# Optimization experiments

Measured on AMD Instinct MI355X. Metric: run time of the kernel, lower is better.

## Reference

```python
import jax, jax.numpy as jnp
import numpy as np

EPS = 1e-07

def setup_inputs() -> dict:
    key = jax.random.key(0)
    k1, k2 = jax.random.split(key)
    B, C = 65536, 1000
    output = jax.random.normal(k1, (B, C), dtype=jnp.float32)
    target = jax.random.randint(k2, (B,), 0, C, dtype=jnp.int64)
    return {"output": output, "target": target}

def reference(output, target):
    B, C = output.shape
    # L2-normalize each row (p=2 norm over class dim) then softmax over classes
    norms = jnp.linalg.norm(output, axis=-1, keepdims=True) + EPS
    probs = jax.nn.softmax(output / norms, axis=1)  # [B, C]
    # per-class mean confidence [C]
    avg_conf = jnp.mean(probs, axis=0)
    # per-class empirical frequency [C] via one-hot-free bincount
    counts = jnp.zeros((C,), dtype=probs.dtype).at[target].add(1.0)
    avg_count = counts / B
    # mean absolute calibration gap over classes (scalar)
    return jnp.mean(jnp.abs(avg_conf - avg_count))
```

## Files before the change

kernel.cpp:

```cpp
#include <hip/hip_runtime.h>
#include <math.h>

#define TPB 512
#define NBLK 1024
#define CCLS 1000

__device__ __forceinline__ float wave_sum64(float x) {
  int t;
  t = __builtin_amdgcn_update_dpp(0, __float_as_int(x), 0x111, 0xf, 0xf, true); x += __int_as_float(t);
  t = __builtin_amdgcn_update_dpp(0, __float_as_int(x), 0x112, 0xf, 0xf, true); x += __int_as_float(t);
  t = __builtin_amdgcn_update_dpp(0, __float_as_int(x), 0x114, 0xf, 0xf, true); x += __int_as_float(t);
  t = __builtin_amdgcn_update_dpp(0, __float_as_int(x), 0x118, 0xf, 0xf, true); x += __int_as_float(t);
  t = __builtin_amdgcn_update_dpp(0, __float_as_int(x), 0x142, 0xa, 0xf, true); x += __int_as_float(t);
  t = __builtin_amdgcn_update_dpp(0, __float_as_int(x), 0x143, 0xc, 0xf, true); x += __int_as_float(t);
  return __int_as_float(__builtin_amdgcn_readlane(__float_as_int(x), 63));
}

__global__ __launch_bounds__(TPB, 8) void mdca_main(const float* __restrict__ X,
                                                    float* __restrict__ g_acc, int B) {
  __shared__ float sacc[1024];
  const int t = threadIdx.x;
  const int lane = t & 63;
  const int wid = blockIdx.x * (TPB / 64) + (t >> 6);
  const int nw = NBLK * (TPB / 64);
  const bool v3 = (lane < 58);

  for (int i = t; i < 1024; i += TPB) sacc[i] = 0.f;

  float acc[16];
  #pragma unroll
  for (int i = 0; i < 16; ++i) acc[i] = 0.f;

  const float4 Z = make_float4(0.f, 0.f, 0.f, 0.f);

  for (int r = wid; r < B; r += nw) {
    const float4* b = reinterpret_cast<const float4*>(X + (size_t)r * CCLS);
    float4 a0 = b[lane];
    float4 a1 = b[64 + lane];
    float4 a2 = b[128 + lane];
    float4 a3 = v3 ? b[192 + lane] : Z;

    float ss = a0.x*a0.x + a0.y*a0.y + a0.z*a0.z + a0.w*a0.w
             + a1.x*a1.x + a1.y*a1.y + a1.z*a1.z + a1.w*a1.w
             + a2.x*a2.x + a2.y*a2.y + a2.z*a2.z + a2.w*a2.w
             + a3.x*a3.x + a3.y*a3.y + a3.z*a3.z + a3.w*a3.w;
    ss = wave_sum64(ss);

    const float inv = 1.0f / (sqrtf(ss) + 1e-7f);

    a0.x=__expf(a0.x*inv); a0.y=__expf(a0.y*inv); a0.z=__expf(a0.z*inv); a0.w=__expf(a0.w*inv);
    a1.x=__expf(a1.x*inv); a1.y=__expf(a1.y*inv); a1.z=__expf(a1.z*inv); a1.w=__expf(a1.w*inv);
    a2.x=__expf(a2.x*inv); a2.y=__expf(a2.y*inv); a2.z=__expf(a2.z*inv); a2.w=__expf(a2.w*inv);
    a3.x=__expf(a3.x*inv); a3.y=__expf(a3.y*inv); a3.z=__expf(a3.z*inv); a3.w=__expf(a3.w*inv);
    if (!v3) a3 = Z;

    float es = a0.x+a0.y+a0.z+a0.w + a1.x+a1.y+a1.z+a1.w
             + a2.x+a2.y+a2.z+a2.w + a3.x+a3.y+a3.z+a3.w;
    es = wave_sum64(es);

    const float invS = 1.0f / es;

    acc[0]  += a0.x*invS;  acc[1]  += a0.y*invS;  acc[2]  += a0.z*invS;  acc[3]  += a0.w*invS;
    acc[4]  += a1.x*invS;  acc[5]  += a1.y*invS;  acc[6]  += a1.z*invS;  acc[7]  += a1.w*invS;
    acc[8]  += a2.x*invS;  acc[9]  += a2.y*invS;  acc[10] += a2.z*invS;  acc[11] += a2.w*invS;
    acc[12] += a3.x*invS;  acc[13] += a3.y*invS;  acc[14] += a3.z*invS;  acc[15] += a3.w*invS;
  }

  __syncthreads();
  #pragma unroll
  for (int k = 0; k < 4; ++k)
    #pragma unroll
    for (int j = 0; j < 4; ++j)
      atomicAdd(&sacc[k * 256 + lane * 4 + j], acc[k * 4 + j]);
  __syncthreads();
  #pragma unroll
  for (int j = 0; j < 2; ++j) {
    int c = t * 2 + j;
    if (c < CCLS) atomicAdd(&g_acc[c], sacc[c]);
  }
}

__global__ __launch_bounds__(256) void mdca_count(const int* __restrict__ tgt,
                                                  float* __restrict__ g_cnt, int B) {
  __shared__ int scnt[CCLS];
  for (int i = threadIdx.x; i < CCLS; i += 256) scnt[i] = 0;
  __syncthreads();
  for (int i = blockIdx.x * 256 + threadIdx.x; i < B; i += gridDim.x * 256)
    atomicAdd(&scnt[tgt[i]], 1);
  __syncthreads();
  for (int i = threadIdx.x; i < CCLS; i += 256) {
    int v = scnt[i];
    if (v) atomicAdd(&g_cnt[i], (float)v);
  }
}

__global__ __launch_bounds__(256) void mdca_final(const float* __restrict__ g_acc,
                                                  const float* __restrict__ g_cnt,
                                                  float* __restrict__ out, int B) {
  __shared__ float s_r[4];
  int t = threadIdx.x;
  float invB = 1.0f / (float)B;
  float s = 0.f;
  for (int c = t; c < CCLS; c += 256)
    s += fabsf((g_acc[c] - g_cnt[c]) * invB);
  #pragma unroll
  for (int off = 32; off > 0; off >>= 1) s += __shfl_down(s, off, 64);
  if ((t & 63) == 0) s_r[t >> 6] = s;
  __syncthreads();
  if (t == 0) out[0] = (s_r[0] + s_r[1] + s_r[2] + s_r[3]) / (float)CCLS;
}

extern "C" void kernel_launch(void* const* d_in, const int* in_sizes, int n_in,
                              void* d_out, int out_size, void* d_ws, size_t ws_size,
                              hipStream_t stream) {
  const float* X = (const float*)d_in[0];
  const int* tgt = (const int*)d_in[1];
  const int B = in_sizes[1];

  float* g_acc = (float*)d_ws;
  float* g_cnt = g_acc + 1024;

  hipMemsetAsync(d_ws, 0, 2048 * sizeof(float), stream);

  mdca_count<<<32, 256, 0, stream>>>(tgt, g_cnt, B);
  mdca_main<<<NBLK, TPB, 0, stream>>>(X, g_acc, B);
  mdca_final<<<1, 256, 0, stream>>>(g_acc, g_cnt, (float*)d_out, B);
}
```

Measured before the change: 380.3 us.

## Fuse count, main and final kernels with last-block reduction; use exp2

```diff
diff --git a/kernel.cpp b/kernel.cpp
--- a/kernel.cpp
+++ b/kernel.cpp
@@ -16,9 +16,25 @@
   return __int_as_float(__builtin_amdgcn_readlane(__float_as_int(x), 63));
 }
 
-__global__ __launch_bounds__(TPB, 8) void mdca_main(const float* __restrict__ X,
-                                                    float* __restrict__ g_acc, int B) {
+__device__ __forceinline__ float fexp2(float x) {
+#if __has_builtin(__builtin_amdgcn_exp2f)
+  return __builtin_amdgcn_exp2f(x);
+#else
+  return exp2f(x);
+#endif
+}
+
+__device__ __forceinline__ float coherent_load(const float* p) {
+  return __hip_atomic_load(p, __ATOMIC_RELAXED, __HIP_MEMORY_SCOPE_AGENT);
+}
+
+__global__ __launch_bounds__(TPB, 8) void mdca_fused(const float* __restrict__ X,
+                                                     const int* __restrict__ tgt,
+                                                     float* __restrict__ g_acc,
+                                                     float* __restrict__ out, int B) {
   __shared__ float sacc[1024];
+  __shared__ float s_r[TPB / 64];
+  __shared__ int s_last;
   const int t = threadIdx.x;
   const int lane = t & 63;
   const int wid = blockIdx.x * (TPB / 64) + (t >> 6);
@@ -46,12 +62,12 @@
              + a3.x*a3.x + a3.y*a3.y + a3.z*a3.z + a3.w*a3.w;
     ss = wave_sum64(ss);
 
-    const float inv = 1.0f / (sqrtf(ss) + 1e-7f);
+    const float il2 = 1.44269504f / (sqrtf(ss) + 1e-7f);
 
-    a0.x=__expf(a0.x*inv); a0.y=__expf(a0.y*inv); a0.z=__expf(a0.z*inv); a0.w=__expf(a0.w*inv);
-    a1.x=__expf(a1.x*inv); a1.y=__expf(a1.y*inv); a1.z=__expf(a1.z*inv); a1.w=__expf(a1.w*inv);
-    a2.x=__expf(a2.x*inv); a2.y=__expf(a2.y*inv); a2.z=__expf(a2.z*inv); a2.w=__expf(a2.w*inv);
-    a3.x=__expf(a3.x*inv); a3.y=__expf(a3.y*inv); a3.z=__expf(a3.z*inv); a3.w=__expf(a3.w*inv);
+    a0.x=fexp2(a0.x*il2); a0.y=fexp2(a0.y*il2); a0.z=fexp2(a0.z*il2); a0.w=fexp2(a0.w*il2);
+    a1.x=fexp2(a1.x*il2); a1.y=fexp2(a1.y*il2); a1.z=fexp2(a1.z*il2); a1.w=fexp2(a1.w*il2);
+    a2.x=fexp2(a2.x*il2); a2.y=fexp2(a2.y*il2); a2.z=fexp2(a2.z*il2); a2.w=fexp2(a2.w*il2);
+    a3.x=fexp2(a3.x*il2); a3.y=fexp2(a3.y*il2); a3.z=fexp2(a3.z*il2); a3.w=fexp2(a3.w*il2);
     if (!v3) a3 = Z;
 
     float es = a0.x+a0.y+a0.z+a0.w + a1.x+a1.y+a1.z+a1.w
@@ -72,42 +88,43 @@
     #pragma unroll
     for (int j = 0; j < 4; ++j)
       atomicAdd(&sacc[k * 256 + lane * 4 + j], acc[k * 4 + j]);
+
+  if (t < 64) {
+    for (int i = blockIdx.x * 64 + t; i < B; i += NBLK * 64)
+      atomicAdd(&sacc[tgt[i]], -1.0f);
+  }
   __syncthreads();
+
   #pragma unroll
   for (int j = 0; j < 2; ++j) {
     int c = t * 2 + j;
     if (c < CCLS) atomicAdd(&g_acc[c], sacc[c]);
   }
-}
 
-__global__ __launch_bounds__(256) void mdca_count(const int* __restrict__ tgt,
-                                                  float* __restrict__ g_cnt, int B) {
-  __shared__ int scnt[CCLS];
-  for (int i = threadIdx.x; i < CCLS; i += 256) scnt[i] = 0;
   __syncthreads();
-  for (int i = blockIdx.x * 256 + threadIdx.x; i < B; i += gridDim.x * 256)
-    atomicAdd(&scnt[tgt[i]], 1);
+  if (t == 0) {
+    __threadfence();
+    unsigned* dcnt = (unsigned*)(g_acc + 1000);
+    unsigned old = __hip_atomic_fetch_add(dcnt, 1u, __ATOMIC_ACQ_REL,
+                                          __HIP_MEMORY_SCOPE_AGENT);
+    s_last = (old == (unsigned)(NBLK - 1));
+  }
   __syncthreads();
-  for (int i = threadIdx.x; i < CCLS; i += 256) {
-    int v = scnt[i];
-    if (v) atomicAdd(&g_cnt[i], (float)v);
+  if (s_last) {
+    const float invB = 1.0f / (float)B;
+    float s = 0.f;
+    for (int c = t; c < CCLS; c += TPB)
+      s += fabsf(coherent_load(&g_acc[c]) * invB);
+    s = wave_sum64(s);
+    if (lane == 0) s_r[t >> 6] = s;
+    __syncthreads();
+    if (t == 0) {
+      float tot = 0.f;
+      #pragma unroll
+      for (int w = 0; w < TPB / 64; ++w) tot += s_r[w];
+      out[0] = tot / (float)CCLS;
+    }
   }
-}
-
-__global__ __launch_bounds__(256) void mdca_final(const float* __restrict__ g_acc,
-                                                  const float* __restrict__ g_cnt,
-                                                  float* __restrict__ out, int B) {
-  __shared__ float s_r[4];
-  int t = threadIdx.x;
-  float invB = 1.0f / (float)B;
-  float s = 0.f;
-  for (int c = t; c < CCLS; c += 256)
-    s += fabsf((g_acc[c] - g_cnt[c]) * invB);
-  #pragma unroll
-  for (int off = 32; off > 0; off >>= 1) s += __shfl_down(s, off, 64);
-  if ((t & 63) == 0) s_r[t >> 6] = s;
-  __syncthreads();
-  if (t == 0) out[0] = (s_r[0] + s_r[1] + s_r[2] + s_r[3]) / (float)CCLS;
 }
 
 extern "C" void kernel_launch(void* const* d_in, const int* in_sizes, int n_in,
@@ -118,11 +135,7 @@
   const int B = in_sizes[1];
 
   float* g_acc = (float*)d_ws;
-  float* g_cnt = g_acc + 1024;
 
-  hipMemsetAsync(d_ws, 0, 2048 * sizeof(float), stream);
-
-  mdca_count<<<32, 256, 0, stream>>>(tgt, g_cnt, B);
-  mdca_main<<<NBLK, TPB, 0, stream>>>(X, g_acc, B);
-  mdca_final<<<1, 256, 0, stream>>>(g_acc, g_cnt, (float*)d_out, B);
+  hipMemsetAsync(d_ws, 0, 1024 * sizeof(float), stream);
+  mdca_fused<<<NBLK, TPB, 0, stream>>>(X, tgt, g_acc, (float*)d_out, B);
 }
```

New measurement: 437.4 us. 1.15x slower.
